# Performance work log

Measured on AMD Instinct MI355X. Metric: run time of the kernel, lower is better.

Reference implementation:

```python
import jax, jax.numpy as jnp
import numpy as np
import math

D_MODEL = 256
D_STATE = 16
D_CONV = 4
EXPAND = 2
N_HEADS = 4
D_INNER = EXPAND * D_MODEL          # 512
DT_RANK = (D_MODEL + 15) // 16      # 16
B_SZ, SEQ = 4, 2048


def setup_inputs() -> dict:
    key = jax.random.key(0)
    ks = jax.random.split(key, 12)
    rn = lambda i, shp, sc=0.02: jax.random.normal(ks[i], shp, dtype=jnp.float32) * sc
    x = jax.random.normal(ks[0], (B_SZ, SEQ, D_MODEL), dtype=jnp.float32)
    return dict(
        x=x,
        ln_g=jnp.ones((D_MODEL,), jnp.float32),
        ln_b=jnp.zeros((D_MODEL,), jnp.float32),
        W_in=rn(1, (D_MODEL, 2 * D_INNER)),
        conv_w=rn(2, (D_INNER, D_CONV), 0.1),
        conv_b=jnp.zeros((D_INNER,), jnp.float32),
        W_xproj=rn(3, (D_INNER, DT_RANK + 2 * D_STATE)),
        W_dt=rn(4, (DT_RANK, D_INNER), 0.1),
        b_dt=jnp.full((D_INNER,), -4.6, jnp.float32),  # softplus ~ 0.01 init
        A_log=jnp.log(jnp.tile(jnp.arange(1, D_STATE + 1, dtype=jnp.float32), (D_INNER, 1))),
        Dp=jnp.ones((D_INNER,), jnp.float32),
        W_out_m=rn(5, (D_INNER, D_MODEL)),
        W_qkv=rn(6, (D_MODEL, 3 * D_MODEL)),
        b_qkv=jnp.zeros((3 * D_MODEL,), jnp.float32),
        W_o=rn(7, (D_MODEL, D_MODEL)),
        b_o=jnp.zeros((D_MODEL,), jnp.float32),
        W_gate=rn(8, (2 * D_MODEL, D_MODEL)),
        b_gate=jnp.zeros((D_MODEL,), jnp.float32),
    )


def _sssd_forward(x, ln_g, ln_b, W_in, conv_w, conv_b, W_xproj, W_dt, b_dt,
                  A_log, Dp, W_out_m, W_qkv, b_qkv, W_o, b_o, W_gate, b_gate):
    B, L, D = x.shape
    # LayerNorm
    mu = x.mean(-1, keepdims=True)
    var = x.var(-1, keepdims=True)
    xn = (x - mu) * jax.lax.rsqrt(var + 1e-5) * ln_g + ln_b

    # ---- Mamba branch ----
    xz = xn @ W_in                      # (B,L,2*D_INNER)
    xm, z = jnp.split(xz, 2, axis=-1)
    # causal depthwise conv1d (kernel D_CONV)
    xp = jnp.pad(xm, ((0, 0), (D_CONV - 1, 0), (0, 0)))
    xc = conv_b + sum(xp[:, k:k + L, :] * conv_w[:, k] for k in range(D_CONV))
    xc = jax.nn.silu(xc)
    dbl = xc @ W_xproj                  # (B,L,DT_RANK+2*D_STATE)
    dt_in = dbl[..., :DT_RANK]
    Bm = dbl[..., DT_RANK:DT_RANK + D_STATE]
    Cm = dbl[..., DT_RANK + D_STATE:]
    dt = jax.nn.softplus(dt_in @ W_dt + b_dt)   # (B,L,D_INNER)
    A = -jnp.exp(A_log)                 # (D_INNER, D_STATE)

    def step(h, inp):
        x_t, dt_t, B_t, C_t = inp       # (B,Din),(B,Din),(B,N),(B,N)
        dA = jnp.exp(dt_t[..., None] * A)               # (B,Din,N)
        h = dA * h + (dt_t * x_t)[..., None] * B_t[:, None, :]
        y = jnp.einsum('bdn,bn->bd', h, C_t)
        return h, y

    h0 = jnp.zeros((B, D_INNER, D_STATE), x.dtype)
    xs = (jnp.swapaxes(xc, 0, 1), jnp.swapaxes(dt, 0, 1),
          jnp.swapaxes(Bm, 0, 1), jnp.swapaxes(Cm, 0, 1))
    _, ys = jax.lax.scan(step, h0, xs)
    y = jnp.swapaxes(ys, 0, 1) + xc * Dp
    y = y * jax.nn.silu(z)
    ssm_out = y @ W_out_m               # (B,L,D)

    # ---- MHSA branch (eval: no dropout) ----
    hd = D // N_HEADS
    qkv = xn @ W_qkv + b_qkv
    q, k, v = jnp.split(qkv, 3, axis=-1)
    sh = lambda t: t.reshape(B, L, N_HEADS, hd).transpose(0, 2, 1, 3)
    q, k, v = sh(q), sh(k), sh(v)
    scores = jnp.einsum('bhqd,bhkd->bhqk', q, k) * (1.0 / math.sqrt(hd))
    attn = jax.nn.softmax(scores, axis=-1)
    o = jnp.einsum('bhqk,bhkd->bhqd', attn, v).transpose(0, 2, 1, 3).reshape(B, L, D)
    attn_out = o @ W_o + b_o

    # ---- sigmoid gate fusion ----
    gate = jax.nn.sigmoid(jnp.concatenate([ssm_out, attn_out], axis=-1) @ W_gate + b_gate)
    fused = gate * ssm_out + (1.0 - gate) * attn_out
    return x + fused


def reference(x, ln_g, ln_b, W_in, conv_w, conv_b, W_xproj, W_dt, b_dt,
              A_log, Dp, W_out_m, W_qkv, b_qkv, W_o, b_o, W_gate, b_gate):
    return _sssd_forward(x, ln_g, ln_b, W_in, conv_w, conv_b, W_xproj, W_dt, b_dt,
                         A_log, Dp, W_out_m, W_qkv, b_qkv, W_o, b_o, W_gate, b_gate)
```

## Files before the change

### kernel.cpp

```cpp
#include <hip/hip_runtime.h>
#include <math.h>

#define B_SZ 4
#define SEQ 2048
#define DM 256
#define DI 512
#define DS 16
#define DTR 16
#define NH 4
#define HD 64
#define T_TOK (B_SZ*SEQ)
#define NCH 64
#define CL (SEQ/NCH)
#define QSCALE 0.18033688f

typedef short bf16x8 __attribute__((ext_vector_type(8)));
typedef float f32x4  __attribute__((ext_vector_type(4)));
typedef float f32x16 __attribute__((ext_vector_type(16)));
typedef unsigned short u16;

__device__ __forceinline__ float sigmoidf_(float x){ return 1.f/(1.f+__expf(-x)); }
__device__ __forceinline__ u16 f2bf(float x){
  unsigned int u = __float_as_uint(x);
  u += 0x7fffu + ((u>>16)&1u);
  return (u16)(u>>16);
}
__device__ __forceinline__ float bf2f(u16 u){ return __uint_as_float(((unsigned)u)<<16); }
__device__ __forceinline__ unsigned cvt_pk_bf16(float lo, float hi){
  unsigned r;
  asm("v_cvt_pk_bf16_f32 %0, %1, %2" : "=v"(r) : "v"(lo), "v"(hi));
  return r;
}

struct TcvtArgs {
  const float* src[6];
  u16* dst[6];
  int K[6];
  int Nvalid[6];
  int Npad[6];
};
__global__ __launch_bounds__(256) void tcvt_all(TcvtArgs a) {
  int wi = blockIdx.z;
  int K = a.K[wi], Nv = a.Nvalid[wi], Np = a.Npad[wi];
  int k0 = blockIdx.x*64, n0 = blockIdx.y*64;
  if (k0 >= K || n0 >= Np) return;
  __shared__ u16 tile[64][65];
  const float* src = a.src[wi];
  u16* dst = a.dst[wi];
  int tn = threadIdx.x & 63, tq = threadIdx.x >> 6;
#pragma unroll
  for (int j=0;j<16;++j){
    int kk = j*4 + tq;
    int n = n0 + tn;
    tile[tn][kk] = (n < Nv) ? f2bf(src[(size_t)(k0+kk)*Nv + n]) : (u16)0;
  }
  __syncthreads();
#pragma unroll
  for (int j=0;j<16;++j){
    int nn = j*4 + tq;
    dst[(size_t)(n0+nn)*K + k0 + tn] = tile[nn][tn];
  }
}

__global__ __launch_bounds__(256) void ln_kernel(const float* __restrict__ x,
    const float* __restrict__ g, const float* __restrict__ b,
    u16* __restrict__ xn_bf) {
  int wid = threadIdx.x >> 6;
  int lane = threadIdx.x & 63;
  int token = blockIdx.x*4 + wid;
  const float* xr = x + (size_t)token*DM;
  float4 v = *(const float4*)&xr[lane*4];
  float s  = v.x+v.y+v.z+v.w;
  float ss = v.x*v.x+v.y*v.y+v.z*v.z+v.w*v.w;
  for (int m=1;m<64;m<<=1){ s += __shfl_xor(s,m); ss += __shfl_xor(ss,m); }
  float mu  = s * (1.f/DM);
  float var = ss*(1.f/DM) - mu*mu;
  float rs  = rsqrtf(var + 1e-5f);
  float4 gv = *(const float4*)&g[lane*4];
  float4 bv = *(const float4*)&b[lane*4];
  uint2 o;
  o.x = cvt_pk_bf16((v.x-mu)*rs*gv.x + bv.x, (v.y-mu)*rs*gv.y + bv.y);
  o.y = cvt_pk_bf16((v.z-mu)*rs*gv.z + bv.z, (v.w-mu)*rs*gv.w + bv.w);
  *(uint2*)&xn_bf[(size_t)token*DM + lane*4] = o;
}

template<int ACT>
__global__ __launch_bounds__(256) void gemm_mfma(const u16* __restrict__ A,
    const u16* __restrict__ Wt, const float* __restrict__ bias,
    float* __restrict__ C, u16* __restrict__ Cbf, int K, int ldc, int nvalid,
    int qcols, float qscale, const float* __restrict__ xres,
    const float* __restrict__ cat2, u16* __restrict__ vTout) {
  __shared__ u16 lds[12288];
  int tid = threadIdx.x;
  int m0 = blockIdx.y*128, n0 = blockIdx.x*64;
  int w = tid>>6, l = tid&63, lq = l&15, lg = l>>4;
  int wm = w>>1, wn = w&1;
  f32x4 acc[4][2] = {};
  for (int k0 = 0; k0 < K; k0 += 64) {
#pragma unroll
    for (int i=0;i<4;++i){
      int gid = i*256 + tid;
      int row = gid>>3, g = gid&7;
      *(bf16x8*)&lds[row*64 + ((g ^ (row&7))*8)] =
          *(const bf16x8*)&A[(size_t)(m0+row)*K + k0 + g*8];
    }
#pragma unroll
    for (int i=0;i<2;++i){
      int gid = i*256 + tid;
      int row = gid>>3, g = gid&7;
      *(bf16x8*)&lds[8192 + row*64 + ((g ^ (row&7))*8)] =
          *(const bf16x8*)&Wt[(size_t)(n0+row)*K + k0 + g*8];
    }
    __syncthreads();
#pragma unroll
    for (int ks=0;ks<2;++ks){
      bf16x8 af[4], bfv[2];
#pragma unroll
      for (int mi=0;mi<4;++mi){
        int row = wm*64 + mi*16 + lq;
        af[mi] = *(bf16x8*)&lds[row*64 + (((ks*4+lg) ^ (row&7))*8)];
      }
#pragma unroll
      for (int nj=0;nj<2;++nj){
        int row = wn*32 + nj*16 + lq;
        bfv[nj] = *(bf16x8*)&lds[8192 + row*64 + (((ks*4+lg) ^ (row&7))*8)];
      }
#pragma unroll
      for (int mi=0;mi<4;++mi)
#pragma unroll
        for (int nj=0;nj<2;++nj)
          acc[mi][nj] = __builtin_amdgcn_mfma_f32_16x16x32_bf16(af[mi], bfv[nj], acc[mi][nj], 0,0,0);
    }
    __syncthreads();
  }
#pragma unroll
  for (int mi=0;mi<4;++mi){
#pragma unroll
    for (int nj=0;nj<2;++nj){
#pragma unroll
      for (int r=0;r<4;++r){
        int row = m0 + wm*64 + mi*16 + lg*4 + r;
        int col = n0 + wn*32 + nj*16 + lq;
        if (col < nvalid) {
          float v = acc[mi][nj][r];
          if (bias) v += bias[col];
          if (col < qcols) v *= qscale;
          if (ACT==2) {
            float g = sigmoidf_(v);
            float sv = cat2[(size_t)row*512 + col];
            float av = cat2[(size_t)row*512 + 256 + col];
            C[(size_t)row*256 + col] = xres[(size_t)row*256 + col] + g*sv + (1.f-g)*av;
          } else if (ACT==3) {
            Cbf[(size_t)row*ldc + col] = f2bf(v);
            if (col >= 512) {
              int bb = row>>11, ll = row&2047;
              int hh = (col-512)>>6, dd = (col-512)&63;
              vTout[(((size_t)(bb*4+hh))*64 + dd)*SEQ + ll] = f2bf(v);
            }
          } else {
            if (ACT==1) v = sigmoidf_(v);
            if (C)   C[(size_t)row*ldc + col] = v;
            if (Cbf) Cbf[(size_t)row*ldc + col] = f2bf(v);
          }
        }
      }
    }
  }
}

__global__ __launch_bounds__(256) void conv_kernel(const u16* __restrict__ xzb,
    const float* __restrict__ cw, const float* __restrict__ cb,
    u16* __restrict__ xc_bf) {
  int idx = blockIdx.x*256 + threadIdx.x;
  int d2 = (idx & 255)*2;
  int t = idx >> 8;
  int l = t & (SEQ-1);
  float acc0 = cb[d2], acc1 = cb[d2+1];
  float4 wA = *(const float4*)&cw[d2*4];
  float4 wB = *(const float4*)&cw[d2*4+4];
  const u16* base = xzb + (size_t)t*1024 + d2;
  ushort2 v;
  if (l>=3){ v = *(const ushort2*)&base[-3*1024]; acc0 += bf2f(v.x)*wA.x; acc1 += bf2f(v.y)*wB.x; }
  if (l>=2){ v = *(const ushort2*)&base[-2*1024]; acc0 += bf2f(v.x)*wA.y; acc1 += bf2f(v.y)*wB.y; }
  if (l>=1){ v = *(const ushort2*)&base[-1*1024]; acc0 += bf2f(v.x)*wA.z; acc1 += bf2f(v.y)*wB.z; }
  v = *(const ushort2*)&base[0];
  acc0 += bf2f(v.x)*wA.w; acc1 += bf2f(v.y)*wB.w;
  float r0 = acc0 * sigmoidf_(acc0);
  float r1 = acc1 * sigmoidf_(acc1);
  *(unsigned*)&xc_bf[(size_t)t*DI + d2] = cvt_pk_bf16(r0, r1);
}

__global__ __launch_bounds__(256) void dt_kernel(const float* __restrict__ dbl,
    const float* __restrict__ Wdt, const float* __restrict__ bdt,
    float* __restrict__ dt) {
  __shared__ float sdbl[4][16];
  int wid = threadIdx.x>>6, lane = threadIdx.x&63;
  int token = blockIdx.x*4 + wid;
  if (lane < 16) sdbl[wid][lane] = dbl[(size_t)token*48 + lane];
  __syncthreads();
  float din[16];
#pragma unroll
  for (int k=0;k<16;++k) din[k] = sdbl[wid][k];
#pragma unroll
  for (int r=0;r<8;++r){
    int d = lane + r*64;
    float acc = bdt[d];
#pragma unroll
    for (int k=0;k<16;++k) acc += din[k]*Wdt[k*DI+d];
    float sp = (acc > 20.f) ? acc : log1pf(__expf(acc));
    dt[(size_t)token*DI+d] = sp;
  }
}

__global__ __launch_bounds__(512) void scan_p1(const u16* __restrict__ xc_bf,
    const float* __restrict__ dt, const float* __restrict__ dbl,
    const float* __restrict__ A_log, float* __restrict__ Pws, float* __restrict__ Hws) {
  __shared__ float sB[CL][16];
  int d = threadIdx.x;
  int bc = blockIdx.x;
  int b = bc >> 6, c = bc & 63;
  {
    int t = threadIdx.x >> 4, n = threadIdx.x & 15;
    sB[t][n] = dbl[((size_t)b*SEQ + c*CL + t)*48 + DTR + n];
  }
  __syncthreads();
  float An[16];
#pragma unroll
  for (int i=0;i<4;++i){
    float4 a = *(const float4*)&A_log[d*16 + i*4];
    An[i*4+0] = -__expf(a.x); An[i*4+1] = -__expf(a.y);
    An[i*4+2] = -__expf(a.z); An[i*4+3] = -__expf(a.w);
  }
  float h[16] = {};
  float P[16];
#pragma unroll
  for (int n=0;n<16;++n) P[n] = 1.f;
  size_t tok = (size_t)b*SEQ + c*CL;
  for (int t=0;t<CL;++t,++tok){
    float dtv = dt[tok*DI+d];
    float xcv = bf2f(xc_bf[tok*DI+d]);
    float u = dtv*xcv;
    float4 B0 = *(float4*)&sB[t][0];
    float4 B1 = *(float4*)&sB[t][4];
    float4 B2 = *(float4*)&sB[t][8];
    float4 B3 = *(float4*)&sB[t][12];
    float Bv[16] = {B0.x,B0.y,B0.z,B0.w,B1.x,B1.y,B1.z,B1.w,
                    B2.x,B2.y,B2.z,B2.w,B3.x,B3.y,B3.z,B3.w};
#pragma unroll
    for (int n=0;n<16;++n){
      float e = __expf(dtv*An[n]);
      P[n] *= e;
      h[n] = e*h[n] + u*Bv[n];
    }
  }
  size_t base = (((size_t)b*NCH + c)*DI + d)*16;
#pragma unroll
  for (int n=0;n<16;++n){ Pws[base+n] = P[n]; Hws[base+n] = h[n]; }
}

__global__ __launch_bounds__(256) void scan_combine(const float* __restrict__ Pws,
    const float* __restrict__ Hws, float* __restrict__ H0ws) {
  int gid = blockIdx.x*256 + threadIdx.x;
  int b  = gid >> 13;
  int dn = gid & 8191;
  float h0 = 0.f;
#pragma unroll 4
  for (int c=0;c<NCH;++c){
    size_t idx = ((size_t)(b*NCH+c)<<13) + dn;
    H0ws[idx] = h0;
    h0 = Pws[idx]*h0 + Hws[idx];
  }
}

__global__ __launch_bounds__(512) void scan_p2(const u16* __restrict__ xc_bf,
    const float* __restrict__ dt, const float* __restrict__ dbl,
    const float* __restrict__ A_log, const float* __restrict__ Dp,
    const u16* __restrict__ xzb, const float* __restrict__ H0ws,
    u16* __restrict__ ygate_bf) {
  __shared__ float sBC[CL][32];
  int d = threadIdx.x;
  int bc = blockIdx.x;
  int b = bc >> 6, c = bc & 63;
#pragma unroll
  for (int i=0;i<2;++i){
    int idx = i*512 + threadIdx.x;
    int t = idx >> 5, q = idx & 31;
    sBC[t][q] = dbl[((size_t)b*SEQ + c*CL + t)*48 + DTR + q];
  }
  __syncthreads();
  float An[16];
#pragma unroll
  for (int i=0;i<4;++i){
    float4 a = *(const float4*)&A_log[d*16 + i*4];
    An[i*4+0] = -__expf(a.x); An[i*4+1] = -__expf(a.y);
    An[i*4+2] = -__expf(a.z); An[i*4+3] = -__expf(a.w);
  }
  float Dd = Dp[d];
  float h[16];
  size_t base = (((size_t)b*NCH + c)*DI + d)*16;
#pragma unroll
  for (int i=0;i<4;++i){
    float4 h4 = *(const float4*)&H0ws[base + i*4];
    h[i*4+0]=h4.x; h[i*4+1]=h4.y; h[i*4+2]=h4.z; h[i*4+3]=h4.w;
  }
  size_t tok = (size_t)b*SEQ + c*CL;
  for (int t=0;t<CL;++t,++tok){
    float dtv = dt[tok*DI+d];
    float xcv = bf2f(xc_bf[tok*DI+d]);
    float zv  = bf2f(xzb[tok*1024 + DI + d]);
    float u = dtv*xcv;
    float4 B0 = *(float4*)&sBC[t][0];
    float4 B1 = *(float4*)&sBC[t][4];
    float4 B2 = *(float4*)&sBC[t][8];
    float4 B3 = *(float4*)&sBC[t][12];
    float4 C0 = *(float4*)&sBC[t][16];
    float4 C1 = *(float4*)&sBC[t][20];
    float4 C2 = *(float4*)&sBC[t][24];
    float4 C3 = *(float4*)&sBC[t][28];
    float Bv[16] = {B0.x,B0.y,B0.z,B0.w,B1.x,B1.y,B1.z,B1.w,
                    B2.x,B2.y,B2.z,B2.w,B3.x,B3.y,B3.z,B3.w};
    float Cv[16] = {C0.x,C0.y,C0.z,C0.w,C1.x,C1.y,C1.z,C1.w,
                    C2.x,C2.y,C2.z,C2.w,C3.x,C3.y,C3.z,C3.w};
    float y = 0.f;
#pragma unroll
    for (int n=0;n<16;++n){
      float e = __expf(dtv*An[n]);
      h[n] = e*h[n] + u*Bv[n];
      y += h[n]*Cv[n];
    }
    y += xcv*Dd;
    ygate_bf[tok*DI + d] = f2bf(y * (zv*sigmoidf_(zv)));
  }
}

__global__ __launch_bounds__(256) void attn_mfma_kernel(const u16* __restrict__ qkvb,
    const u16* __restrict__ vT,
    float* __restrict__ Opart, float* __restrict__ ml) {
  __shared__ u16 lds[8192];
  int H = blockIdx.x + 16*blockIdx.y + 256*(int)blockIdx.z;
  int cx = H & 7, k = H >> 3;
  int xq = k & 15;
  int G  = cx*8 + (k >> 4);
  int bh = G & 15, s = G >> 4;
  int b = bh>>2, h = bh&3;
  int tid = threadIdx.x;
  int w = tid>>6, l = tid&63;
  int lo32 = l & 31;
  int hi = l >> 5;
  size_t bbase = (size_t)b*SEQ;
  size_t vbase = (size_t)bh*HD*SEQ;
  int q0 = xq*128 + w*32;
  int q = q0 + lo32;

  bf16x8 qf[4];
#pragma unroll
  for (int dsl=0; dsl<4; ++dsl)
    qf[dsl] = *(const bf16x8*)&qkvb[(bbase + q)*768 + h*HD + dsl*16 + hi*8];

  float m_ = -1e30f, l_ = 0.f;
  f32x16 oacc[2] = {};

  int srow = tid>>3, sg = tid&7;
  int kt0 = s*8;
  bf16x8 kreg[2], vreg[2];

#define LOADT(kt) { \
  kreg[0] = *(const bf16x8*)&qkvb[(bbase + (size_t)(kt)*64 + srow)*768 + 256 + h*HD + sg*8]; \
  kreg[1] = *(const bf16x8*)&qkvb[(bbase + (size_t)(kt)*64 + srow + 32)*768 + 256 + h*HD + sg*8]; \
  vreg[0] = *(const bf16x8*)&vT[vbase + (size_t)srow*SEQ + (kt)*64 + sg*8]; \
  vreg[1] = *(const bf16x8*)&vT[vbase + (size_t)(srow+32)*SEQ + (kt)*64 + sg*8]; }
#define STORET() { \
  *(bf16x8*)&lds[srow*64 + ((sg ^ (srow&7))*8)] = kreg[0]; \
  *(bf16x8*)&lds[(srow+32)*64 + ((sg ^ ((srow+32)&7))*8)] = kreg[1]; \
  *(bf16x8*)&lds[4096 + srow*64 + ((sg ^ (srow&7))*8)] = vreg[0]; \
  *(bf16x8*)&lds[4096 + (srow+32)*64 + ((sg ^ ((srow+32)&7))*8)] = vreg[1]; }
#define EXCH(X, Y, s_own, s_oth) { \
  unsigned give = (l < 32) ? (Y) : (X); \
  unsigned got = __shfl_xor(give, 32); \
  s_own = (l < 32) ? (X) : got; \
  s_oth = (l < 32) ? got : (Y); }

  LOADT(kt0);
  for (int it=0; it<8; ++it){
    __syncthreads();
    STORET();
    __syncthreads();
    if (it < 7) LOADT(kt0+it+1);

#pragma unroll
    for (int t32=0; t32<2; ++t32){
      f32x16 sacc = {0,0,0,0,0,0,0,0,0,0,0,0,0,0,0,0};
      __builtin_amdgcn_s_setprio(1);
#pragma unroll
      for (int dsl=0; dsl<4; ++dsl){
        int row = t32*32 + lo32;
        bf16x8 kf = *(bf16x8*)&lds[row*64 + (((dsl*2 + hi) ^ (row&7))*8)];
        sacc = __builtin_amdgcn_mfma_f32_32x32x16_bf16(kf, qf[dsl], sacc, 0,0,0);
      }
      __builtin_amdgcn_s_setprio(0);

      float tm = sacc[0];
#pragma unroll
      for (int r=1;r<16;++r) tm = fmaxf(tm, sacc[r]);
      tm = fmaxf(tm, __shfl_xor(tm, 32));
      if (__any(tm - m_ > 8.f)) {
        float mn = fmaxf(m_, tm);
        float sc = exp2f(m_ - mn);
        m_ = mn;
        l_ *= sc;
#pragma unroll
        for (int r=0;r<16;++r){ oacc[0][r] *= sc; oacc[1][r] *= sc; }
      }
      float p[16];
      float ps = 0.f;
#pragma unroll
      for (int r=0;r<16;++r){ p[r] = exp2f(sacc[r] - m_); ps += p[r]; }
      ps += __shfl_xor(ps, 32);
      l_ += ps;

      unsigned A0 = cvt_pk_bf16(p[0],p[1]),  A1 = cvt_pk_bf16(p[2],p[3]);
      unsigned B0 = cvt_pk_bf16(p[4],p[5]),  B1 = cvt_pk_bf16(p[6],p[7]);
      unsigned C0 = cvt_pk_bf16(p[8],p[9]),  C1 = cvt_pk_bf16(p[10],p[11]);
      unsigned D0 = cvt_pk_bf16(p[12],p[13]),D1 = cvt_pk_bf16(p[14],p[15]);
      unsigned s0,s1,s2,s3,s4,s5,s6,s7;
      EXCH(A0,B0,s0,s2); EXCH(A1,B1,s1,s3);
      EXCH(C0,D0,s4,s6); EXCH(C1,D1,s5,s7);
      bf16x8 pf0, pf1;
      ((unsigned*)&pf0)[0]=s0; ((unsigned*)&pf0)[1]=s1; ((unsigned*)&pf0)[2]=s2; ((unsigned*)&pf0)[3]=s3;
      ((unsigned*)&pf1)[0]=s4; ((unsigned*)&pf1)[1]=s5; ((unsigned*)&pf1)[2]=s6; ((unsigned*)&pf1)[3]=s7;

      __builtin_amdgcn_s_setprio(1);
#pragma unroll
      for (int dtile=0; dtile<2; ++dtile){
        int row = dtile*32 + lo32;
        bf16x8 vf0 = *(bf16x8*)&lds[4096 + row*64 + (((t32*4 + 0 + hi) ^ (row&7))*8)];
        bf16x8 vf1 = *(bf16x8*)&lds[4096 + row*64 + (((t32*4 + 2 + hi) ^ (row&7))*8)];
        oacc[dtile] = __builtin_amdgcn_mfma_f32_32x32x16_bf16(vf0, pf0, oacc[dtile], 0,0,0);
        oacc[dtile] = __builtin_amdgcn_mfma_f32_32x32x16_bf16(vf1, pf1, oacc[dtile], 0,0,0);
      }
      __builtin_amdgcn_s_setprio(0);
    }
  }
#undef LOADT
#undef STORET
#undef EXCH

  int sidx = bh*4 + s;
  size_t rb = ((size_t)sidx*SEQ + q)*64;
#pragma unroll
  for (int dtile=0; dtile<2; ++dtile){
#pragma unroll
    for (int rg=0; rg<4; ++rg){
      float4 v4;
      v4.x = oacc[dtile][rg*4+0];
      v4.y = oacc[dtile][rg*4+1];
      v4.z = oacc[dtile][rg*4+2];
      v4.w = oacc[dtile][rg*4+3];
      *(float4*)&Opart[rb + dtile*32 + rg*8 + 4*hi] = v4;
    }
  }
  if (l < 32){
    ml[((size_t)sidx*SEQ + q)*2    ] = m_;
    ml[((size_t)sidx*SEQ + q)*2 + 1] = l_;
  }
}

__global__ __launch_bounds__(256) void attn_merge_kernel(const float* __restrict__ Opart,
    const float* __restrict__ ml, u16* __restrict__ attn_bf) {
  int w = threadIdx.x>>6, lane = threadIdx.x&63;
  int R = blockIdx.x*4 + w;
  int bh = R>>11, q = R&2047;
  float m[4], lv[4];
#pragma unroll
  for (int s=0;s<4;++s){
    m[s]  = ml[((size_t)(bh*4+s)*SEQ + q)*2];
    lv[s] = ml[((size_t)(bh*4+s)*SEQ + q)*2 + 1];
  }
  float ms = fmaxf(fmaxf(m[0],m[1]),fmaxf(m[2],m[3]));
  float o = 0.f, lsum = 0.f;
#pragma unroll
  for (int s=0;s<4;++s){
    float wsc = exp2f(m[s]-ms);
    lsum += wsc*lv[s];
    o += wsc*Opart[((size_t)(bh*4+s)*SEQ + q)*64 + lane];
  }
  size_t token = (size_t)(bh>>2)*SEQ + q;
  attn_bf[token*DM + (bh&3)*HD + lane] = f2bf(o/lsum);
}

extern "C" void kernel_launch(void* const* d_in, const int* in_sizes, int n_in,
                              void* d_out, int out_size, void* d_ws, size_t ws_size,
                              hipStream_t stream) {
  const float* x      = (const float*)d_in[0];
  const float* ln_g   = (const float*)d_in[1];
  const float* ln_b   = (const float*)d_in[2];
  const float* W_in   = (const float*)d_in[3];
  const float* conv_w = (const float*)d_in[4];
  const float* conv_b = (const float*)d_in[5];
  const float* W_xproj= (const float*)d_in[6];
  const float* W_dt   = (const float*)d_in[7];
  const float* b_dt   = (const float*)d_in[8];
  const float* A_log  = (const float*)d_in[9];
  const float* Dp     = (const float*)d_in[10];
  const float* W_out_m= (const float*)d_in[11];
  const float* W_qkv  = (const float*)d_in[12];
  const float* b_qkv  = (const float*)d_in[13];
  const float* W_o    = (const float*)d_in[14];
  const float* b_o    = (const float*)d_in[15];
  const float* W_gate = (const float*)d_in[16];
  const float* b_gate = (const float*)d_in[17];
  float* out = (float*)d_out;

  float* ws = (float*)d_ws;
  u16*   xn_bf   = (u16*)(ws);
  u16*   xzb     = (u16*)(ws + 1048576);
  u16*   qkv_bf  = (u16*)(ws + 9437184);
  u16*   xc_bf   = (u16*)(ws + 12582912);
  float* dblb    = ws + 16777216;
  float* dtb     = ws + 17170432;
  u16*   ygate_bf= (u16*)(ws + 21364736);
  u16*   attn_bf = (u16*)(ws + 23461888);
  float* catb    = ws + 24510464;
  u16*   catb_bf = (u16*)(ws + 28704768);
  float* gateb   = ws + 30801920;
  u16*   Wt_all  = (u16*)(ws + 32899072);
  float* Opart = ws + 1048576;
  float* mlb   = (float*)xn_bf;
  u16*   vTb   = (u16*)gateb;
  float* Pws   = catb;
  float* Hws   = catb + 2097152;
  float* H0ws  = catb + 4194304;

  u16* Wt_in   = Wt_all;
  u16* Wt_qkv  = Wt_all + 262144;
  u16* Wt_out  = Wt_all + 458752;
  u16* Wt_o    = Wt_all + 589824;
  u16* Wt_gate = Wt_all + 655360;
  u16* Wt_xp   = Wt_all + 786432;

  TcvtArgs ta;
  ta.src[0]=W_in;    ta.dst[0]=Wt_in;   ta.K[0]=256; ta.Nvalid[0]=1024; ta.Npad[0]=1024;
  ta.src[1]=W_qkv;   ta.dst[1]=Wt_qkv;  ta.K[1]=256; ta.Nvalid[1]=768;  ta.Npad[1]=768;
  ta.src[2]=W_out_m; ta.dst[2]=Wt_out;  ta.K[2]=512; ta.Nvalid[2]=256;  ta.Npad[2]=256;
  ta.src[3]=W_o;     ta.dst[3]=Wt_o;    ta.K[3]=256; ta.Nvalid[3]=256;  ta.Npad[3]=256;
  ta.src[4]=W_gate;  ta.dst[4]=Wt_gate; ta.K[4]=512; ta.Nvalid[4]=256;  ta.Npad[4]=256;
  ta.src[5]=W_xproj; ta.dst[5]=Wt_xp;   ta.K[5]=512; ta.Nvalid[5]=48;   ta.Npad[5]=64;
  tcvt_all<<<dim3(8,16,6), 256, 0, stream>>>(ta);

  ln_kernel<<<T_TOK/4, 256, 0, stream>>>(x, ln_g, ln_b, xn_bf);
  gemm_mfma<0><<<dim3(16,64), 256, 0, stream>>>(xn_bf, Wt_in, nullptr, nullptr, xzb, 256, 1024, 1024, 0, 1.f, nullptr, nullptr, nullptr);
  gemm_mfma<3><<<dim3(12,64), 256, 0, stream>>>(xn_bf, Wt_qkv, b_qkv, nullptr, qkv_bf, 256, 768, 768, 256, QSCALE, nullptr, nullptr, vTb);
  conv_kernel<<<T_TOK, 256, 0, stream>>>(xzb, conv_w, conv_b, xc_bf);
  gemm_mfma<0><<<dim3(1,64), 256, 0, stream>>>(xc_bf, Wt_xp, nullptr, dblb, nullptr, 512, 48, 48, 0, 1.f, nullptr, nullptr, nullptr);
  dt_kernel<<<T_TOK/4, 256, 0, stream>>>(dblb, W_dt, b_dt, dtb);
  scan_p1<<<B_SZ*NCH, 512, 0, stream>>>(xc_bf, dtb, dblb, A_log, Pws, Hws);
  scan_combine<<<128, 256, 0, stream>>>(Pws, Hws, H0ws);
  scan_p2<<<B_SZ*NCH, 512, 0, stream>>>(xc_bf, dtb, dblb, A_log, Dp, xzb, H0ws, ygate_bf);
  attn_mfma_kernel<<<dim3(16, 16, 4), 256, 0, stream>>>(qkv_bf, vTb, Opart, mlb);
  attn_merge_kernel<<<8192, 256, 0, stream>>>(Opart, mlb, attn_bf);
  gemm_mfma<0><<<dim3(4,64), 256, 0, stream>>>(ygate_bf, Wt_out, nullptr, catb, catb_bf, 512, 512, 256, 0, 1.f, nullptr, nullptr, nullptr);
  gemm_mfma<0><<<dim3(4,64), 256, 0, stream>>>(attn_bf, Wt_o, b_o, catb+256, catb_bf+256, 256, 512, 256, 0, 1.f, nullptr, nullptr, nullptr);
  gemm_mfma<2><<<dim3(4,64), 256, 0, stream>>>(catb_bf, Wt_gate, b_gate, out, nullptr, 512, 256, 256, 0, 1.f, x, catb, nullptr);
}
```

Baseline: 248.7 us.

## Store dt in bf16 and double per-wave query tile in attention kernel

The dt intermediate is written and read as bf16 instead of fp32, halving its memory traffic in dt_kernel and both scan passes, at some precision cost in dt. The attention kernel now gives each wave two 32-query groups, so each K/V tile loaded from LDS feeds twice as many MFMAs, and the grid is halved. This raises register pressure (two sets of Q fragments and accumulators) and cuts the number of blocks, which may lower occupancy.

Measured after the change: 250.9 us. No clear change (+0.9%).

```diff
diff --git a/kernel.cpp b/kernel.cpp
--- a/kernel.cpp
+++ b/kernel.cpp
@@ -192,7 +192,7 @@
 
 __global__ __launch_bounds__(256) void dt_kernel(const float* __restrict__ dbl,
     const float* __restrict__ Wdt, const float* __restrict__ bdt,
-    float* __restrict__ dt) {
+    u16* __restrict__ dt) {
   __shared__ float sdbl[4][16];
   int wid = threadIdx.x>>6, lane = threadIdx.x&63;
   int token = blockIdx.x*4 + wid;
@@ -208,12 +208,12 @@
 #pragma unroll
     for (int k=0;k<16;++k) acc += din[k]*Wdt[k*DI+d];
     float sp = (acc > 20.f) ? acc : log1pf(__expf(acc));
-    dt[(size_t)token*DI+d] = sp;
+    dt[(size_t)token*DI+d] = f2bf(sp);
   }
 }
 
 __global__ __launch_bounds__(512) void scan_p1(const u16* __restrict__ xc_bf,
-    const float* __restrict__ dt, const float* __restrict__ dbl,
+    const u16* __restrict__ dt, const float* __restrict__ dbl,
     const float* __restrict__ A_log, float* __restrict__ Pws, float* __restrict__ Hws) {
   __shared__ float sB[CL][16];
   int d = threadIdx.x;
@@ -237,7 +237,7 @@
   for (int n=0;n<16;++n) P[n] = 1.f;
   size_t tok = (size_t)b*SEQ + c*CL;
   for (int t=0;t<CL;++t,++tok){
-    float dtv = dt[tok*DI+d];
+    float dtv = bf2f(dt[tok*DI+d]);
     float xcv = bf2f(xc_bf[tok*DI+d]);
     float u = dtv*xcv;
     float4 B0 = *(float4*)&sB[t][0];
@@ -273,7 +273,7 @@
 }
 
 __global__ __launch_bounds__(512) void scan_p2(const u16* __restrict__ xc_bf,
-    const float* __restrict__ dt, const float* __restrict__ dbl,
+    const u16* __restrict__ dt, const float* __restrict__ dbl,
     const float* __restrict__ A_log, const float* __restrict__ Dp,
     const u16* __restrict__ xzb, const float* __restrict__ H0ws,
     u16* __restrict__ ygate_bf) {
@@ -305,7 +305,7 @@
   }
   size_t tok = (size_t)b*SEQ + c*CL;
   for (int t=0;t<CL;++t,++tok){
-    float dtv = dt[tok*DI+d];
+    float dtv = bf2f(dt[tok*DI+d]);
     float xcv = bf2f(xc_bf[tok*DI+d]);
     float zv  = bf2f(xzb[tok*1024 + DI + d]);
     float u = dtv*xcv;
@@ -337,10 +337,10 @@
     const u16* __restrict__ vT,
     float* __restrict__ Opart, float* __restrict__ ml) {
   __shared__ u16 lds[8192];
-  int H = blockIdx.x + 16*blockIdx.y + 256*(int)blockIdx.z;
-  int cx = H & 7, k = H >> 3;
-  int xq = k & 15;
-  int G  = cx*8 + (k >> 4);
+  int H = blockIdx.x + 8*blockIdx.y + 128*(int)blockIdx.z;
+  int cx = H & 7, kk = H >> 3;
+  int xq = kk & 7;
+  int G  = cx*8 + (kk >> 3);
   int bh = G & 15, s = G >> 4;
   int b = bh>>2, h = bh&3;
   int tid = threadIdx.x;
@@ -349,16 +349,17 @@
   int hi = l >> 5;
   size_t bbase = (size_t)b*SEQ;
   size_t vbase = (size_t)bh*HD*SEQ;
-  int q0 = xq*128 + w*32;
-  int q = q0 + lo32;
-
-  bf16x8 qf[4];
-#pragma unroll
-  for (int dsl=0; dsl<4; ++dsl)
-    qf[dsl] = *(const bf16x8*)&qkvb[(bbase + q)*768 + h*HD + dsl*16 + hi*8];
-
-  float m_ = -1e30f, l_ = 0.f;
-  f32x16 oacc[2] = {};
+  int q_base = xq*256 + w*64;
+
+  bf16x8 qf[2][4];
+#pragma unroll
+  for (int qg=0; qg<2; ++qg)
+#pragma unroll
+    for (int dsl=0; dsl<4; ++dsl)
+      qf[qg][dsl] = *(const bf16x8*)&qkvb[(bbase + q_base + qg*32 + lo32)*768 + h*HD + dsl*16 + hi*8];
+
+  float m_[2] = {-1e30f,-1e30f}, l_[2] = {0.f,0.f};
+  f32x16 oacc[2][2] = {};
 
   int srow = tid>>3, sg = tid&7;
   int kt0 = s*8;
@@ -389,54 +390,64 @@
 
 #pragma unroll
     for (int t32=0; t32<2; ++t32){
-      f32x16 sacc = {0,0,0,0,0,0,0,0,0,0,0,0,0,0,0,0};
+      int krow = t32*32 + lo32;
+      bf16x8 kf[4];
+#pragma unroll
+      for (int dsl=0; dsl<4; ++dsl)
+        kf[dsl] = *(bf16x8*)&lds[krow*64 + (((dsl*2 + hi) ^ (krow&7))*8)];
+
+      bf16x8 pf[2][2];
+#pragma unroll
+      for (int qg=0; qg<2; ++qg){
+        f32x16 sacc = {0,0,0,0,0,0,0,0,0,0,0,0,0,0,0,0};
+        __builtin_amdgcn_s_setprio(1);
+#pragma unroll
+        for (int dsl=0; dsl<4; ++dsl)
+          sacc = __builtin_amdgcn_mfma_f32_32x32x16_bf16(kf[dsl], qf[qg][dsl], sacc, 0,0,0);
+        __builtin_amdgcn_s_setprio(0);
+
+        float tm = sacc[0];
+#pragma unroll
+        for (int r=1;r<16;++r) tm = fmaxf(tm, sacc[r]);
+        tm = fmaxf(tm, __shfl_xor(tm, 32));
+        if (__any(tm - m_[qg] > 8.f)) {
+          float mn = fmaxf(m_[qg], tm);
+          float sc = exp2f(m_[qg] - mn);
+          m_[qg] = mn;
+          l_[qg] *= sc;
+#pragma unroll
+          for (int r=0;r<16;++r){ oacc[qg][0][r] *= sc; oacc[qg][1][r] *= sc; }
+        }
+        float p[16];
+        float ps = 0.f;
+#pragma unroll
+        for (int r=0;r<16;++r){ p[r] = exp2f(sacc[r] - m_[qg]); ps += p[r]; }
+        ps += __shfl_xor(ps, 32);
+        l_[qg] += ps;
+
+        unsigned A0 = cvt_pk_bf16(p[0],p[1]),  A1 = cvt_pk_bf16(p[2],p[3]);
+        unsigned B0 = cvt_pk_bf16(p[4],p[5]),  B1 = cvt_pk_bf16(p[6],p[7]);
+        unsigned C0 = cvt_pk_bf16(p[8],p[9]),  C1 = cvt_pk_bf16(p[10],p[11]);
+        unsigned D0 = cvt_pk_bf16(p[12],p[13]),D1 = cvt_pk_bf16(p[14],p[15]);
+        unsigned s0,s1,s2,s3,s4,s5,s6,s7;
+        EXCH(A0,B0,s0,s2); EXCH(A1,B1,s1,s3);
+        EXCH(C0,D0,s4,s6); EXCH(C1,D1,s5,s7);
+        ((unsigned*)&pf[qg][0])[0]=s0; ((unsigned*)&pf[qg][0])[1]=s1;
+        ((unsigned*)&pf[qg][0])[2]=s2; ((unsigned*)&pf[qg][0])[3]=s3;
+        ((unsigned*)&pf[qg][1])[0]=s4; ((unsigned*)&pf[qg][1])[1]=s5;
+        ((unsigned*)&pf[qg][1])[2]=s6; ((unsigned*)&pf[qg][1])[3]=s7;
+      }
+
       __builtin_amdgcn_s_setprio(1);
 #pragma unroll
-      for (int dsl=0; dsl<4; ++dsl){
-        int row = t32*32 + lo32;
-        bf16x8 kf = *(bf16x8*)&lds[row*64 + (((dsl*2 + hi) ^ (row&7))*8)];
-        sacc = __builtin_amdgcn_mfma_f32_32x32x16_bf16(kf, qf[dsl], sacc, 0,0,0);
-      }
-      __builtin_amdgcn_s_setprio(0);
-
-      float tm = sacc[0];
-#pragma unroll
-      for (int r=1;r<16;++r) tm = fmaxf(tm, sacc[r]);
-      tm = fmaxf(tm, __shfl_xor(tm, 32));
-      if (__any(tm - m_ > 8.f)) {
-        float mn = fmaxf(m_, tm);
-        float sc = exp2f(m_ - mn);
-        m_ = mn;
-        l_ *= sc;
-#pragma unroll
-        for (int r=0;r<16;++r){ oacc[0][r] *= sc; oacc[1][r] *= sc; }
-      }
-      float p[16];
-      float ps = 0.f;
-#pragma unroll
-      for (int r=0;r<16;++r){ p[r] = exp2f(sacc[r] - m_); ps += p[r]; }
-      ps += __shfl_xor(ps, 32);
-      l_ += ps;
-
-      unsigned A0 = cvt_pk_bf16(p[0],p[1]),  A1 = cvt_pk_bf16(p[2],p[3]);
-      unsigned B0 = cvt_pk_bf16(p[4],p[5]),  B1 = cvt_pk_bf16(p[6],p[7]);
-      unsigned C0 = cvt_pk_bf16(p[8],p[9]),  C1 = cvt_pk_bf16(p[10],p[11]);
-      unsigned D0 = cvt_pk_bf16(p[12],p[13]),D1 = cvt_pk_bf16(p[14],p[15]);
-      unsigned s0,s1,s2,s3,s4,s5,s6,s7;
-      EXCH(A0,B0,s0,s2); EXCH(A1,B1,s1,s3);
-      EXCH(C0,D0,s4,s6); EXCH(C1,D1,s5,s7);
-      bf16x8 pf0, pf1;
-      ((unsigned*)&pf0)[0]=s0; ((unsigned*)&pf0)[1]=s1; ((unsigned*)&pf0)[2]=s2; ((unsigned*)&pf0)[3]=s3;
-      ((unsigned*)&pf1)[0]=s4; ((unsigned*)&pf1)[1]=s5; ((unsigned*)&pf1)[2]=s6; ((unsigned*)&pf1)[3]=s7;
-
-      __builtin_amdgcn_s_setprio(1);
-#pragma unroll
       for (int dtile=0; dtile<2; ++dtile){
-        int row = dtile*32 + lo32;
-        bf16x8 vf0 = *(bf16x8*)&lds[4096 + row*64 + (((t32*4 + 0 + hi) ^ (row&7))*8)];
-        bf16x8 vf1 = *(bf16x8*)&lds[4096 + row*64 + (((t32*4 + 2 + hi) ^ (row&7))*8)];
-        oacc[dtile] = __builtin_amdgcn_mfma_f32_32x32x16_bf16(vf0, pf0, oacc[dtile], 0,0,0);
-        oacc[dtile] = __builtin_amdgcn_mfma_f32_32x32x16_bf16(vf1, pf1, oacc[dtile], 0,0,0);
+        int vrow = dtile*32 + lo32;
+        bf16x8 vf0 = *(bf16x8*)&lds[4096 + vrow*64 + (((t32*4 + 0 + hi) ^ (vrow&7))*8)];
+        bf16x8 vf1 = *(bf16x8*)&lds[4096 + vrow*64 + (((t32*4 + 2 + hi) ^ (vrow&7))*8)];
+        oacc[0][dtile] = __builtin_amdgcn_mfma_f32_32x32x16_bf16(vf0, pf[0][0], oacc[0][dtile], 0,0,0);
+        oacc[0][dtile] = __builtin_amdgcn_mfma_f32_32x32x16_bf16(vf1, pf[0][1], oacc[0][dtile], 0,0,0);
+        oacc[1][dtile] = __builtin_amdgcn_mfma_f32_32x32x16_bf16(vf0, pf[1][0], oacc[1][dtile], 0,0,0);
+        oacc[1][dtile] = __builtin_amdgcn_mfma_f32_32x32x16_bf16(vf1, pf[1][1], oacc[1][dtile], 0,0,0);
       }
       __builtin_amdgcn_s_setprio(0);
     }
@@ -446,22 +457,25 @@
 #undef EXCH
 
   int sidx = bh*4 + s;
-  size_t rb = ((size_t)sidx*SEQ + q)*64;
-#pragma unroll
-  for (int dtile=0; dtile<2; ++dtile){
-#pragma unroll
-    for (int rg=0; rg<4; ++rg){
-      float4 v4;
-      v4.x = oacc[dtile][rg*4+0];
-      v4.y = oacc[dtile][rg*4+1];
-      v4.z = oacc[dtile][rg*4+2];
-      v4.w = oacc[dtile][rg*4+3];
-      *(float4*)&Opart[rb + dtile*32 + rg*8 + 4*hi] = v4;
-    }
-  }
-  if (l < 32){
-    ml[((size_t)sidx*SEQ + q)*2    ] = m_;
-    ml[((size_t)sidx*SEQ + q)*2 + 1] = l_;
+#pragma unroll
+  for (int qg=0; qg<2; ++qg){
+    size_t rb = ((size_t)sidx*SEQ + q_base + qg*32 + lo32)*64;
+#pragma unroll
+    for (int dtile=0; dtile<2; ++dtile){
+#pragma unroll
+      for (int rg=0; rg<4; ++rg){
+        float4 v4;
+        v4.x = oacc[qg][dtile][rg*4+0];
+        v4.y = oacc[qg][dtile][rg*4+1];
+        v4.z = oacc[qg][dtile][rg*4+2];
+        v4.w = oacc[qg][dtile][rg*4+3];
+        *(float4*)&Opart[rb + dtile*32 + rg*8 + 4*hi] = v4;
+      }
+    }
+    if (l < 32){
+      ml[((size_t)sidx*SEQ + q_base + qg*32 + lo32)*2    ] = m_[qg];
+      ml[((size_t)sidx*SEQ + q_base + qg*32 + lo32)*2 + 1] = l_[qg];
+    }
   }
 }
 
@@ -517,7 +531,7 @@
   u16*   qkv_bf  = (u16*)(ws + 9437184);
   u16*   xc_bf   = (u16*)(ws + 12582912);
   float* dblb    = ws + 16777216;
-  float* dtb     = ws + 17170432;
+  u16*   dtb     = (u16*)(ws + 17170432);
   u16*   ygate_bf= (u16*)(ws + 21364736);
   u16*   attn_bf = (u16*)(ws + 23461888);
   float* catb    = ws + 24510464;
@@ -556,7 +570,7 @@
   scan_p1<<<B_SZ*NCH, 512, 0, stream>>>(xc_bf, dtb, dblb, A_log, Pws, Hws);
   scan_combine<<<128, 256, 0, stream>>>(Pws, Hws, H0ws);
   scan_p2<<<B_SZ*NCH, 512, 0, stream>>>(xc_bf, dtb, dblb, A_log, Dp, xzb, H0ws, ygate_bf);
-  attn_mfma_kernel<<<dim3(16, 16, 4), 256, 0, stream>>>(qkv_bf, vTb, Opart, mlb);
+  attn_mfma_kernel<<<dim3(8, 16, 4), 256, 0, stream>>>(qkv_bf, vTb, Opart, mlb);
   attn_merge_kernel<<<8192, 256, 0, stream>>>(Opart, mlb, attn_bf);
   gemm_mfma<0><<<dim3(4,64), 256, 0, stream>>>(ygate_bf, Wt_out, nullptr, catb, catb_bf, 512, 512, 256, 0, 1.f, nullptr, nullptr, nullptr);
   gemm_mfma<0><<<dim3(4,64), 256, 0, stream>>>(attn_bf, Wt_o, b_o, catb+256, catb_bf+256, 256, 512, 256, 0, 1.f, nullptr, nullptr, nullptr);
```
